# Kernel tuning notes

Hardware: AMD Instinct MI355X
Metric: run time of the kernel (lower is better)

## Reference

```python
import jax, jax.numpy as jnp
from jax import lax
import numpy as np

B, T, D, H, OUT = 128, 1024, 3, 512, 26


def setup_inputs() -> dict:
    key = jax.random.key(0)
    ks = jax.random.split(key, 8)
    s_in = 1.0 / np.sqrt(D)
    s_h = 1.0 / np.sqrt(H)
    return {
        "x": jax.random.normal(ks[0], (B, T, D), jnp.float32),
        # layer 0: gate order [i, f, z, o], W:(4H,in), R:(4H,H), b:(4H,)
        "W0": jax.random.normal(ks[1], (4 * H, D), jnp.float32) * s_in,
        "R0": jax.random.normal(ks[2], (4 * H, H), jnp.float32) * s_h,
        "b0": jnp.zeros((4 * H,), jnp.float32),
        # layer 1
        "W1": jax.random.normal(ks[3], (4 * H, H), jnp.float32) * s_h,
        "R1": jax.random.normal(ks[4], (4 * H, H), jnp.float32) * s_h,
        "b1": jnp.zeros((4 * H,), jnp.float32),
        # final linear head
        "fc_w": jax.random.normal(ks[5], (OUT, H), jnp.float32) * s_h,
        "fc_b": jnp.zeros((OUT,), jnp.float32),
    }


def _slstm_layer(xp, R):
    """sLSTM with exponential gating + stabilizer/normalizer states.
    xp: (B, T, 4H) precomputed input projections (incl. bias). Returns h: (B, T, H).
    """
    Bn, Tn, H4 = xp.shape
    Hh = H4 // 4

    def step(carry, g_in):
        h, c, n, m = carry
        g = g_in + h @ R.T                      # (B, 4H)
        i_pre, f_pre, z_pre, o_pre = jnp.split(g, 4, axis=-1)
        m_new = jnp.maximum(f_pre + m, i_pre)   # stabilizer (log-space)
        i_g = jnp.exp(i_pre - m_new)            # stabilized exp input gate
        f_g = jnp.exp(f_pre + m - m_new)        # stabilized exp forget gate
        c_new = f_g * c + i_g * jnp.tanh(z_pre)
        n_new = f_g * n + i_g                   # normalizer state
        h_new = jax.nn.sigmoid(o_pre) * c_new / jnp.maximum(n_new, 1e-6)
        return (h_new, c_new, n_new, m_new), h_new

    z = jnp.zeros((Bn, Hh), xp.dtype)
    init = (z, z, z, z)
    _, hs = lax.scan(step, init, jnp.swapaxes(xp, 0, 1))  # (T, B, H)
    return jnp.swapaxes(hs, 0, 1)


def reference(x, W0, R0, b0, W1, R1, b1, fc_w, fc_b):
    # layer 0 (input projections done as one big parallel GEMM)
    xp0 = jnp.einsum("btd,gd->btg", x, W0) + b0
    h1 = _slstm_layer(xp0, R0)
    # layer 1 (inter-layer dropout is identity at eval)
    xp1 = jnp.einsum("bth,gh->btg", h1, W1) + b1
    h2 = _slstm_layer(xp1, R1)
    # last-step hidden -> linear head (dropout identity at eval)
    last = h2[:, -1, :]                         # (B, H)
    return last @ fc_w.T + fc_b                 # (B, OUT)
```

## Files before the change

### kernel.cpp

```cpp
#include <hip/hip_runtime.h>
#include <hip/hip_bf16.h>

typedef _Float16 f16x8 __attribute__((ext_vector_type(8)));
typedef float f32x4 __attribute__((ext_vector_type(4)));
typedef unsigned long long u64;

#define B_   128
#define T_   1024
#define H_   512
#define P_   32
#define HC_  16
#define MB_  32
#define NC_  8
#define NW_  4
#define SPIN_BOUND (1 << 20)

#define FRAG_MT 8192

#define WS_HEXHI  0ull
#define WS_HEXLO  524288ull
#define WS_FLAGR  1048576ull
#define WS_FLAGX  1081344ull
#define WS_XCC    1097728ull
#define WS_MECH   1098752ull
#define WS_PROBE  1099776ull
#define WS_ZEROL  1100800ull
#define WS_XT     1100800ull
#define WS_HLAST  2673664ull
#define WS_H1HI   2935808ull
#define WS_H1LO   137153536ull
#define WS_NEED_SMALL 137153536ull

#define MFMA(a, b, c) __builtin_amdgcn_mfma_f32_16x16x32_f16((a), (b), (c), 0, 0, 0)

#define LD8C(FLAGS, D, P0, P1)                                                  \
    asm volatile(                                                               \
        "global_load_dwordx4 %0, %8, off " FLAGS "\n\t"                         \
        "global_load_dwordx4 %1, %8, off offset:1024 " FLAGS "\n\t"             \
        "global_load_dwordx4 %2, %8, off offset:2048 " FLAGS "\n\t"             \
        "global_load_dwordx4 %3, %8, off offset:3072 " FLAGS "\n\t"             \
        "global_load_dwordx4 %4, %9, off " FLAGS "\n\t"                         \
        "global_load_dwordx4 %5, %9, off offset:1024 " FLAGS "\n\t"             \
        "global_load_dwordx4 %6, %9, off offset:2048 " FLAGS "\n\t"             \
        "global_load_dwordx4 %7, %9, off offset:3072 " FLAGS "\n\t"             \
        "s_waitcnt vmcnt(0)"                                                    \
        : "=&v"(D[0][0]), "=&v"(D[1][0]), "=&v"(D[2][0]), "=&v"(D[3][0]),       \
          "=&v"(D[0][1]), "=&v"(D[1][1]), "=&v"(D[2][1]), "=&v"(D[3][1])        \
        : "v"(P0), "v"(P1)                                                      \
        : "memory")

__device__ __forceinline__ unsigned ald4(const unsigned* p) {
    return __hip_atomic_load(p, __ATOMIC_RELAXED, __HIP_MEMORY_SCOPE_AGENT);
}
__device__ __forceinline__ void ast4(void* p, unsigned v) {
    __hip_atomic_store((unsigned*)p, v, __ATOMIC_RELAXED, __HIP_MEMORY_SCOPE_AGENT);
}
__device__ __forceinline__ void st4_plain(unsigned* p, unsigned v) {
    asm volatile("global_store_dword %0, %1, off" :: "v"(p), "v"(v) : "memory");
}
__device__ __forceinline__ unsigned ld4_sc1(const unsigned* p) {
    unsigned r;
    asm volatile("global_load_dword %0, %1, off sc1\n\ts_waitcnt vmcnt(0)"
                 : "=v"(r) : "v"(p) : "memory");
    return r;
}
__device__ __forceinline__ void st16_plain(void* p, f16x8 v) {
    asm volatile("global_store_dwordx4 %0, %1, off" :: "v"(p), "v"(v) : "memory");
}
__device__ __forceinline__ void st16_ic(void* p, f16x8 v) {
    asm volatile("global_store_dwordx4 %0, %1, off sc0 sc1" :: "v"(p), "v"(v) : "memory");
}
__device__ __forceinline__ unsigned short f16bits(_Float16 h) {
    union { _Float16 f; unsigned short s; } u; u.f = h; return u.s;
}
__device__ __forceinline__ void heat(unsigned v) {
    float a = (float)(v & 7u) + 1.0f;
    #pragma unroll
    for (int i = 0; i < 16; ++i)
        asm volatile("v_fmac_f32 %0, %1, %2" : "+v"(a) : "v"(1.000001f), "v"(a));
    asm volatile("" :: "v"(a));
}
__device__ __forceinline__ int swz(int cidx) { return cidx ^ ((cidx >> 3) & 7); }

__global__ __launch_bounds__(256)
void xt_kernel(const float* __restrict__ x, float* __restrict__ xT) {
    int idx = blockIdx.x * 256 + threadIdx.x;
    if (idx < B_ * T_ * 3) {
        int d = idx % 3, rest = idx / 3;
        int t = rest % T_, b = rest / T_;
        xT[((size_t)t * B_ + b) * 3 + d] = x[idx];
    }
}

__global__ __launch_bounds__(256, 1)
void fused_slstm(const float* __restrict__ xT,
                 const float* __restrict__ W0, const float* __restrict__ R0,
                 const float* __restrict__ b0v,
                 const float* __restrict__ W1, const float* __restrict__ R1,
                 const float* __restrict__ b1v,
                 _Float16* __restrict__ hexFhi, _Float16* __restrict__ hexFlo,
                 unsigned* __restrict__ flagR, unsigned* __restrict__ flagX,
                 unsigned* __restrict__ xccbuf, unsigned* __restrict__ mech,
                 unsigned* __restrict__ probe,
                 _Float16* __restrict__ h1Fhi, _Float16* __restrict__ h1Flo,
                 float* __restrict__ hlast)
{
    constexpr int LDSH = 4 * 16 * 64 * 8;
    __shared__ _Float16 lds[2 * LDSH];
    __shared__ f32x4 bufA[512], bufB[512];
    __shared__ unsigned tbuf32[256];
    __shared__ int verdLds, mechLds, fastLds;

    const int tid  = threadIdx.x;
    const int lane = tid & 63;
    const int wid  = tid >> 6;
    const int l15  = lane & 15;
    const int l4   = lane >> 4;
    const int kg8  = l4 * 8;
    const int c    = blockIdx.x & 7;
    const int p    = blockIdx.x >> 3;
    const bool isL2 = (c >= 4);
    const int g    = c & 3;
    const int b0g  = g * MB_;

    const float* Rg  = isL2 ? R1 : R0;
    const float* bgp = isL2 ? b1v : b0v;

    {
        const int q = wid;
        const int grow = q * H_ + p * HC_ + l15;
        const float* rsrc = Rg + (size_t)grow * H_ + kg8;
        for (int kt = 0; kt < 16; ++kt) {
            const float* s = rsrc + kt * 32;
            _Float16* dhi = &lds[((q * 16 + kt) * 64 + lane) * 8];
            _Float16* dlo = dhi + LDSH;
            if (!isL2) {
                #pragma unroll
                for (int j = 0; j < 8; ++j) {
                    float v = s[j];
                    _Float16 h = (_Float16)v;
                    dhi[j] = h;
                    dlo[j] = (_Float16)(v - (float)h);
                }
            } else {
                const float* ws2 = W1 + (size_t)grow * H_ + kt * 32 + kg8;
                #pragma unroll
                for (int j = 0; j < 8; ++j) {
                    dhi[j] = (_Float16)s[j];
                    dlo[j] = (_Float16)ws2[j];
                }
            }
        }
    }

    {
        unsigned myxcc;
        asm volatile("s_getreg_b32 %0, hwreg(20, 0, 32)" : "=s"(myxcc));
        if (tid == 0) ast4(xccbuf + blockIdx.x, 0x100u | (myxcc & 0xFFu));
        if (wid == 0) {
            const unsigned* xp = xccbuf + ((lane & 31) * 8 + c);
            unsigned v = 0;
            int ok = 0;
            for (int it = 0; it < SPIN_BOUND; ++it) {
                v = ald4(xp);
                if (__ballot(v >= 0x100u) == ~0ull) { ok = 1; break; }
                __builtin_amdgcn_s_sleep(2);
            }
            unsigned ref = (unsigned)__shfl((int)v, 0);
            bool alleq = ok && (__ballot((v & 0xFFu) == (ref & 0xFFu)) == ~0ull);
            unsigned o = 0;
            int ok2 = 0;
            const unsigned* op = xccbuf + (c ^ 1);
            for (int it = 0; it < SPIN_BOUND; ++it) {
                o = ald4(op);
                if (o >= 0x100u) { ok2 = 1; break; }
                __builtin_amdgcn_s_sleep(2);
            }
            bool cand = alleq && ok2 && ((o & 0xFFu) != (ref & 0xFFu));
            if (lane == 0) verdLds = cand ? 1 : 0;
        }
    }
    __syncthreads();
    const bool candFast = (verdLds != 0);

    if (candFast && p == 0 && tid == 0) {
        for (unsigned k = 1; k <= 3; ++k) {
            st4_plain(probe + c * 32, k);
            asm volatile("s_waitcnt vmcnt(0)" ::: "memory");
            for (int s = 0; s < 32; ++s) __builtin_amdgcn_s_sleep(127);
        }
    }
    if (candFast && wid == 0) {
        unsigned first = 0xFFFFFFFFu;
        int got = 0;
        for (int it = 0; it < (1 << 16); ++it) {
            unsigned v = ld4_sc1(probe + c * 32);
            if (first == 0xFFFFFFFFu) first = v;
            if (v >= 3u) { got = 1; break; }
            __builtin_amdgcn_s_sleep(2);
        }
        if (p != 0 && first >= 3u) got = 0;
        if (lane == 0) mechLds = got;
    }
    __syncthreads();
    const int saw = candFast ? mechLds : 0;

    if (tid == 0) ast4(mech + blockIdx.x, 0x100u | (unsigned)(saw & 1));
    if (wid == 0) {
        const unsigned* mp = mech + ((lane & 31) * 8 + c);
        unsigned v = 0;
        int ok = 0;
        for (int it = 0; it < SPIN_BOUND; ++it) {
            v = ald4(mp);
            if (__ballot(v >= 0x100u) == ~0ull) { ok = 1; break; }
            __builtin_amdgcn_s_sleep(2);
        }
        bool allsaw = ok && (__ballot((v & 1u) != 0u) == ~0ull);
        if (lane == 0) fastLds = (candFast && allsaw) ? 1 : 0;
    }

    const int colIdx = tid & 15;
    const int col    = p * HC_ + colIdx;
    const int row0   = tid >> 4;
    float bb[4], w0r[4][3];
    #pragma unroll
    for (int q = 0; q < 4; ++q) bb[q] = bgp[q * H_ + col];
    if (!isL2) {
        #pragma unroll
        for (int q = 0; q < 4; ++q)
            #pragma unroll
            for (int d = 0; d < 3; ++d)
                w0r[q][d] = W0[(size_t)(q * H_ + col) * 3 + d];
    }
    float cS[2] = {0.f, 0.f}, nS[2] = {0.f, 0.f}, mS[2] = {0.f, 0.f};

    const int kt0 = wid * 4;
    int dead = 0;

    __syncthreads();
    const bool fast = (fastLds != 0);

    for (int t = 0; t < T_; ++t) {
        float xa[2][3];
        if (!isL2) {
            #pragma unroll
            for (int h = 0; h < 2; ++h) {
                const float* xp = xT + ((size_t)t * B_ + b0g + row0 + h * 16) * 3;
                xa[h][0] = xp[0]; xa[h][1] = xp[1]; xa[h][2] = xp[2];
            }
        }

        f32x4 acc[2][4];
        #pragma unroll
        for (int mt = 0; mt < 2; ++mt)
            #pragma unroll
            for (int q = 0; q < 4; ++q) { f32x4 z = {0.f,0.f,0.f,0.f}; acc[mt][q] = z; }

        if (isL2) {
            if (!dead) {
                const unsigned* fx = flagX + ((size_t)(g * 32 + (lane & 31)) << 5);
                int it = 0;
                for (;;) {
                    unsigned v = fast ? ld4_sc1(fx) : ald4(fx);
                    if (__ballot(v >= (unsigned)(t + 1)) == ~0ull) break;
                    if (++it > SPIN_BOUND) { dead = 1; break; }
                    heat(v);
                }
            }
            asm volatile("" ::: "memory");
            f16x8 xh[4][2];
            const size_t tb = (((size_t)t * 4 + g) * 2) * FRAG_MT + kt0 * 512 + lane * 8;
            const _Float16* q0 = h1Fhi + tb;
            const _Float16* q1 = h1Fhi + tb + FRAG_MT;
            LD8C("sc0 sc1", xh, q0, q1);
            #pragma unroll
            for (int k = 0; k < 4; ++k)
                #pragma unroll
                for (int q = 0; q < 4; ++q) {
                    f16x8 w = *(const f16x8*)&lds[LDSH + ((q * 16 + kt0 + k) * 64 + lane) * 8];
                    acc[0][q] = MFMA(xh[k][0], w, acc[0][q]);
                    acc[1][q] = MFMA(xh[k][1], w, acc[1][q]);
                }
        }

        if (t > 0 && !dead) {
            const unsigned* fr = flagR + ((size_t)(c * 32 + (lane & 31)) << 5);
            int it = 0;
            for (;;) {
                unsigned v = fast ? ld4_sc1(fr) : ald4(fr);
                if (__ballot(v >= (unsigned)t) == ~0ull) break;
                if (++it > SPIN_BOUND) { dead = 1; break; }
                heat(v);
            }
            asm volatile("" ::: "memory");
        }

        f16x8 ah[4][2];
        {
            const size_t hb = (((size_t)(t & 1) * NC_ + c) * 2) * FRAG_MT + kt0 * 512 + lane * 8;
            const _Float16* ph0 = hexFhi + hb;
            const _Float16* ph1 = hexFhi + hb + FRAG_MT;
            if (fast) { LD8C("sc1", ah, ph0, ph1); }
            else      { LD8C("sc0 sc1", ah, ph0, ph1); }
        }
        #pragma unroll
        for (int k = 0; k < 4; ++k)
            #pragma unroll
            for (int q = 0; q < 4; ++q) {
                f16x8 rh = *(const f16x8*)&lds[((q * 16 + kt0 + k) * 64 + lane) * 8];
                acc[0][q] = MFMA(ah[k][0], rh, acc[0][q]);
                acc[1][q] = MFMA(ah[k][1], rh, acc[1][q]);
                if (!isL2) {
                    f16x8 rlo = *(const f16x8*)&lds[LDSH + ((q * 16 + kt0 + k) * 64 + lane) * 8];
                    acc[0][q] = MFMA(ah[k][0], rlo, acc[0][q]);
                    acc[1][q] = MFMA(ah[k][1], rlo, acc[1][q]);
                }
            }

        if (wid == 1) {
            #pragma unroll
            for (int mt = 0; mt < 2; ++mt)
                #pragma unroll
                for (int q = 0; q < 4; ++q)
                    bufA[swz((mt * 4 + q) * 64 + lane)] = acc[mt][q];
        } else if (wid == 3) {
            #pragma unroll
            for (int mt = 0; mt < 2; ++mt)
                #pragma unroll
                for (int q = 0; q < 4; ++q)
                    bufB[swz((mt * 4 + q) * 64 + lane)] = acc[mt][q];
        }
        __syncthreads();
        if (wid == 2) {
            #pragma unroll
            for (int mt = 0; mt < 2; ++mt)
                #pragma unroll
                for (int q = 0; q < 4; ++q) {
                    const int s = swz((mt * 4 + q) * 64 + lane);
                    f32x4 v = bufA[s]; v += acc[mt][q]; bufA[s] = v;
                }
        } else if (wid == 0) {
            #pragma unroll
            for (int mt = 0; mt < 2; ++mt)
                #pragma unroll
                for (int q = 0; q < 4; ++q) {
                    const int s = swz((mt * 4 + q) * 64 + lane);
                    f32x4 v = bufB[s]; v += acc[mt][q]; bufB[s] = v;
                }
        }
        __syncthreads();

        const float* fA = (const float*)bufA;
        const float* fB = (const float*)bufB;
        unsigned pk[2];
        #pragma unroll
        for (int h = 0; h < 2; ++h) {
            float gq[4];
            #pragma unroll
            for (int q = 0; q < 4; ++q) {
                const int cidx = (h * 4 + q) * 64 + (row0 >> 2) * 16 + colIdx;
                const int w = swz(cidx) * 4 + (row0 & 3);
                float e = fA[w] + fB[w] + bb[q];
                if (!isL2)
                    e += w0r[q][0]*xa[h][0] + w0r[q][1]*xa[h][1] + w0r[q][2]*xa[h][2];
                gq[q] = e;
            }
            float iv = gq[0], fv = gq[1], zv = gq[2], ov = gq[3];
            float fm = fv + mS[h];
            float mn = fmaxf(fm, iv);
            float ig = __expf(iv - mn);
            float fg = __expf(fm - mn);
            float zc = fminf(fmaxf(zv, -15.f), 15.f);
            float e2 = __expf(2.f * zc);
            float th = (e2 - 1.f) / (e2 + 1.f);
            cS[h] = fg * cS[h] + ig * th;
            nS[h] = fg * nS[h] + ig;
            mS[h] = mn;
            float sg = 1.f / (1.f + __expf(-ov));
            float hv = sg * cS[h] / fmaxf(nS[h], 1e-6f);

            if (isL2 && t == T_ - 1)
                hlast[(size_t)(b0g + row0 + h * 16) * H_ + col] = hv;

            unsigned self = (unsigned)f16bits((_Float16)hv);
            unsigned part = (unsigned)__shfl_xor((int)(self << 16), 1) >> 16;
            pk[h] = (self & 0xffffu) | ((unsigned)part << 16);
        }

        if (!(colIdx & 1)) {
            const int fl4i = colIdx >> 3;
            const int cj   = (colIdx & 7) >> 1;
            #pragma unroll
            for (int h = 0; h < 2; ++h)
                tbuf32[((h * 2 + fl4i) * 16 + row0) * 4 + cj] = pk[h];
        }
        __syncthreads();

        if (wid == 0) {
            const f16x8* tv = (const f16x8*)tbuf32;
            f16x8 vh = tv[lane & 63];
            const int mt   = lane >> 5;
            const int fl4i = (lane >> 4) & 1;
            const int row  = lane & 15;
            const int flg  = row + 16 * ((p & 1) * 2 + fl4i);
            const size_t tail = (size_t)(p >> 1) * 512 + (size_t)flg * 8;
            const size_t feh = (((size_t)((t + 1) & 1) * NC_ + c) * 2 + mt) * FRAG_MT + tail;
            if (fast) st16_plain(hexFhi + feh, vh);
            else      st16_ic(hexFhi + feh, vh);
            asm volatile("s_waitcnt vmcnt(0)" ::: "memory");
            if (lane == 0) {
                unsigned* frp = flagR + ((size_t)(c * 32 + p) << 5);
                if (fast) st4_plain(frp, (unsigned)(t + 1));
                else      ast4(frp, (unsigned)(t + 1));
                if (!isL2) ast4(flagX + ((size_t)(c * 32 + p) << 5), (unsigned)t);
            }
            if (!isL2) {
                const size_t fex = (((size_t)t * 4 + g) * 2 + mt) * FRAG_MT + tail;
                st16_ic(h1Fhi + fex, vh);
            }
        }
    }

    if (!isL2) {
        asm volatile("s_waitcnt vmcnt(0)" ::: "memory");
        __syncthreads();
        if (tid == 0) ast4(flagX + ((size_t)(c * 32 + p) << 5), (unsigned)(T_ + 1));
    }
}

#define OUT_ 26
__global__ __launch_bounds__(64)
void fc_kernel(const float* __restrict__ hlast, const float* __restrict__ fcw,
               const float* __restrict__ fcb, float* __restrict__ out)
{
    int b = blockIdx.x, oo = threadIdx.x;
    if (oo < OUT_) {
        const float4* hv = reinterpret_cast<const float4*>(hlast + (size_t)b * H_);
        const float4* wv = reinterpret_cast<const float4*>(fcw + (size_t)oo * H_);
        float s = fcb[oo];
        #pragma unroll 4
        for (int k = 0; k < H_ / 4; ++k) {
            float4 h4 = hv[k], w4 = wv[k];
            s += h4.x * w4.x + h4.y * w4.y + h4.z * w4.z + h4.w * w4.w;
        }
        out[(size_t)b * OUT_ + oo] = s;
    }
}

extern "C" void kernel_launch(void* const* d_in, const int* in_sizes, int n_in,
                              void* d_out, int out_size, void* d_ws, size_t ws_size,
                              hipStream_t stream) {
    const float* x   = (const float*)d_in[0];
    const float* W0  = (const float*)d_in[1];
    const float* R0  = (const float*)d_in[2];
    const float* b0  = (const float*)d_in[3];
    const float* W1  = (const float*)d_in[4];
    const float* R1  = (const float*)d_in[5];
    const float* b1  = (const float*)d_in[6];
    const float* fcw = (const float*)d_in[7];
    const float* fcb = (const float*)d_in[8];
    float* out = (float*)d_out;

    if (ws_size < WS_NEED_SMALL) return;

    char* ws = (char*)d_ws;
    _Float16* hexFhi = (_Float16*)(ws + WS_HEXHI);
    _Float16* hexFlo = (_Float16*)(ws + WS_HEXLO);
    unsigned* flagR  = (unsigned*)(ws + WS_FLAGR);
    unsigned* flagX  = (unsigned*)(ws + WS_FLAGX);
    unsigned* xccb   = (unsigned*)(ws + WS_XCC);
    unsigned* mech   = (unsigned*)(ws + WS_MECH);
    unsigned* probe  = (unsigned*)(ws + WS_PROBE);
    float*    xTp    = (float*)(ws + WS_XT);
    float*    hlast  = (float*)(ws + WS_HLAST);
    _Float16* h1Fhi  = (_Float16*)(ws + WS_H1HI);
    _Float16* h1Flo  = (_Float16*)(ws + WS_H1LO);

    hipMemsetAsync(ws, 0, WS_ZEROL, stream);
    xt_kernel<<<(B_ * T_ * 3 + 255) / 256, 256, 0, stream>>>(x, xTp);
    fused_slstm<<<NC_ * P_, NW_ * 64, 0, stream>>>(xTp, W0, R0, b0, W1, R1, b1,
                                                   hexFhi, hexFlo, flagR, flagX,
                                                   xccb, mech, probe,
                                                   h1Fhi, h1Flo, hlast);
    fc_kernel<<<B_, 64, 0, stream>>>(hlast, fcw, fcb, out);
}
```

Measured before the change: 3.881 ms.

## Split recurrent MFMA across warps by gate pairs and write hidden state directly

Warps are regrouped so each pair covers half the K range for two of the four gates, instead of each warp covering a quarter of K for all gates. Each warp now writes its partial sums straight into one of two LDS buffers, which removes a serial add stage and one block barrier per timestep. The LDS transpose staging buffer is also dropped: threads write packed fp16 hidden values to global memory as scattered dword stores, replacing a single wave's 16-byte stores. The trade is that each warp issues twice as many global fragment loads per step, and the global stores become many small writes.

```diff
diff --git a/kernel.cpp b/kernel.cpp
--- a/kernel.cpp
+++ b/kernel.cpp
@@ -33,20 +33,30 @@
 
 #define MFMA(a, b, c) __builtin_amdgcn_mfma_f32_16x16x32_f16((a), (b), (c), 0, 0, 0)
 
-#define LD8C(FLAGS, D, P0, P1)                                                  \
+#define LD16C(FLAGS, D, DB, P0, P1, P2, P3)                                     \
     asm volatile(                                                               \
-        "global_load_dwordx4 %0, %8, off " FLAGS "\n\t"                         \
-        "global_load_dwordx4 %1, %8, off offset:1024 " FLAGS "\n\t"             \
-        "global_load_dwordx4 %2, %8, off offset:2048 " FLAGS "\n\t"             \
-        "global_load_dwordx4 %3, %8, off offset:3072 " FLAGS "\n\t"             \
-        "global_load_dwordx4 %4, %9, off " FLAGS "\n\t"                         \
-        "global_load_dwordx4 %5, %9, off offset:1024 " FLAGS "\n\t"             \
-        "global_load_dwordx4 %6, %9, off offset:2048 " FLAGS "\n\t"             \
-        "global_load_dwordx4 %7, %9, off offset:3072 " FLAGS "\n\t"             \
+        "global_load_dwordx4 %0, %16, off " FLAGS "\n\t"                        \
+        "global_load_dwordx4 %1, %16, off offset:1024 " FLAGS "\n\t"            \
+        "global_load_dwordx4 %2, %16, off offset:2048 " FLAGS "\n\t"            \
+        "global_load_dwordx4 %3, %16, off offset:3072 " FLAGS "\n\t"            \
+        "global_load_dwordx4 %4, %17, off " FLAGS "\n\t"                        \
+        "global_load_dwordx4 %5, %17, off offset:1024 " FLAGS "\n\t"            \
+        "global_load_dwordx4 %6, %17, off offset:2048 " FLAGS "\n\t"            \
+        "global_load_dwordx4 %7, %17, off offset:3072 " FLAGS "\n\t"            \
+        "global_load_dwordx4 %8, %18, off " FLAGS "\n\t"                        \
+        "global_load_dwordx4 %9, %18, off offset:1024 " FLAGS "\n\t"            \
+        "global_load_dwordx4 %10, %18, off offset:2048 " FLAGS "\n\t"           \
+        "global_load_dwordx4 %11, %18, off offset:3072 " FLAGS "\n\t"           \
+        "global_load_dwordx4 %12, %19, off " FLAGS "\n\t"                       \
+        "global_load_dwordx4 %13, %19, off offset:1024 " FLAGS "\n\t"           \
+        "global_load_dwordx4 %14, %19, off offset:2048 " FLAGS "\n\t"           \
+        "global_load_dwordx4 %15, %19, off offset:3072 " FLAGS "\n\t"           \
         "s_waitcnt vmcnt(0)"                                                    \
         : "=&v"(D[0][0]), "=&v"(D[1][0]), "=&v"(D[2][0]), "=&v"(D[3][0]),       \
-          "=&v"(D[0][1]), "=&v"(D[1][1]), "=&v"(D[2][1]), "=&v"(D[3][1])        \
-        : "v"(P0), "v"(P1)                                                      \
+          "=&v"(D[0][1]), "=&v"(D[1][1]), "=&v"(D[2][1]), "=&v"(D[3][1]),       \
+          "=&v"(DB[0][0]), "=&v"(DB[1][0]), "=&v"(DB[2][0]), "=&v"(DB[3][0]),   \
+          "=&v"(DB[0][1]), "=&v"(DB[1][1]), "=&v"(DB[2][1]), "=&v"(DB[3][1])    \
+        : "v"(P0), "v"(P1), "v"(P2), "v"(P3)                                    \
         : "memory")
 
 __device__ __forceinline__ unsigned ald4(const unsigned* p) {
@@ -63,12 +73,6 @@
     asm volatile("global_load_dword %0, %1, off sc1\n\ts_waitcnt vmcnt(0)"
                  : "=v"(r) : "v"(p) : "memory");
     return r;
-}
-__device__ __forceinline__ void st16_plain(void* p, f16x8 v) {
-    asm volatile("global_store_dwordx4 %0, %1, off" :: "v"(p), "v"(v) : "memory");
-}
-__device__ __forceinline__ void st16_ic(void* p, f16x8 v) {
-    asm volatile("global_store_dwordx4 %0, %1, off sc0 sc1" :: "v"(p), "v"(v) : "memory");
 }
 __device__ __forceinline__ unsigned short f16bits(_Float16 h) {
     union { _Float16 f; unsigned short s; } u; u.f = h; return u.s;
@@ -108,7 +112,6 @@
     constexpr int LDSH = 4 * 16 * 64 * 8;
     __shared__ _Float16 lds[2 * LDSH];
     __shared__ f32x4 bufA[512], bufB[512];
-    __shared__ unsigned tbuf32[256];
     __shared__ int verdLds, mechLds, fastLds;
 
     const int tid  = threadIdx.x;
@@ -222,6 +225,10 @@
     const int colIdx = tid & 15;
     const int col    = p * HC_ + colIdx;
     const int row0   = tid >> 4;
+    const int fkt  = col >> 5;
+    const int fl4s = (col >> 3) & 3;
+    const int fj   = col & 7;
+    const size_t tail = (size_t)fkt * 512 + ((size_t)row0 + 16 * fl4s) * 8 + fj;
     float bb[4], w0r[4][3];
     #pragma unroll
     for (int q = 0; q < 4; ++q) bb[q] = bgp[q * H_ + col];
@@ -234,7 +241,9 @@
     }
     float cS[2] = {0.f, 0.f}, nS[2] = {0.f, 0.f}, mS[2] = {0.f, 0.f};
 
-    const int kt0 = wid * 4;
+    const int gp  = wid & 1;
+    const int kh  = wid >> 1;
+    const int kt0 = kh * 8;
     int dead = 0;
 
     __syncthreads();
@@ -250,11 +259,11 @@
             }
         }
 
-        f32x4 acc[2][4];
+        f32x4 acc[2][2];
         #pragma unroll
         for (int mt = 0; mt < 2; ++mt)
             #pragma unroll
-            for (int q = 0; q < 4; ++q) { f32x4 z = {0.f,0.f,0.f,0.f}; acc[mt][q] = z; }
+            for (int qq = 0; qq < 2; ++qq) { f32x4 z = {0.f,0.f,0.f,0.f}; acc[mt][qq] = z; }
 
         if (isL2) {
             if (!dead) {
@@ -268,19 +277,22 @@
                 }
             }
             asm volatile("" ::: "memory");
-            f16x8 xh[4][2];
+            f16x8 xh[8][2];
             const size_t tb = (((size_t)t * 4 + g) * 2) * FRAG_MT + kt0 * 512 + lane * 8;
             const _Float16* q0 = h1Fhi + tb;
             const _Float16* q1 = h1Fhi + tb + FRAG_MT;
-            LD8C("sc0 sc1", xh, q0, q1);
-            #pragma unroll
-            for (int k = 0; k < 4; ++k)
+            LD16C("sc0 sc1", xh, (xh + 4), q0, q1, (q0 + 2048), (q1 + 2048));
+            #pragma unroll
+            for (int k = 0; k < 8; ++k) {
+                const int kt = kt0 + k;
                 #pragma unroll
-                for (int q = 0; q < 4; ++q) {
-                    f16x8 w = *(const f16x8*)&lds[LDSH + ((q * 16 + kt0 + k) * 64 + lane) * 8];
-                    acc[0][q] = MFMA(xh[k][0], w, acc[0][q]);
-                    acc[1][q] = MFMA(xh[k][1], w, acc[1][q]);
+                for (int qq = 0; qq < 2; ++qq) {
+                    const int q = gp * 2 + qq;
+                    f16x8 w = *(const f16x8*)&lds[LDSH + ((q * 16 + kt) * 64 + lane) * 8];
+                    acc[0][qq] = MFMA(xh[k][0], w, acc[0][qq]);
+                    acc[1][qq] = MFMA(xh[k][1], w, acc[1][qq]);
                 }
+            }
         }
 
         if (t > 0 && !dead) {
@@ -295,58 +307,38 @@
             asm volatile("" ::: "memory");
         }
 
-        f16x8 ah[4][2];
+        f16x8 ah[8][2];
         {
             const size_t hb = (((size_t)(t & 1) * NC_ + c) * 2) * FRAG_MT + kt0 * 512 + lane * 8;
             const _Float16* ph0 = hexFhi + hb;
             const _Float16* ph1 = hexFhi + hb + FRAG_MT;
-            if (fast) { LD8C("sc1", ah, ph0, ph1); }
-            else      { LD8C("sc0 sc1", ah, ph0, ph1); }
+            if (fast) { LD16C("sc1", ah, (ah + 4), ph0, ph1, (ph0 + 2048), (ph1 + 2048)); }
+            else      { LD16C("sc0 sc1", ah, (ah + 4), ph0, ph1, (ph0 + 2048), (ph1 + 2048)); }
         }
         #pragma unroll
-        for (int k = 0; k < 4; ++k)
-            #pragma unroll
-            for (int q = 0; q < 4; ++q) {
-                f16x8 rh = *(const f16x8*)&lds[((q * 16 + kt0 + k) * 64 + lane) * 8];
-                acc[0][q] = MFMA(ah[k][0], rh, acc[0][q]);
-                acc[1][q] = MFMA(ah[k][1], rh, acc[1][q]);
+        for (int k = 0; k < 8; ++k) {
+            const int kt = kt0 + k;
+            #pragma unroll
+            for (int qq = 0; qq < 2; ++qq) {
+                const int q = gp * 2 + qq;
+                f16x8 rh = *(const f16x8*)&lds[((q * 16 + kt) * 64 + lane) * 8];
+                acc[0][qq] = MFMA(ah[k][0], rh, acc[0][qq]);
+                acc[1][qq] = MFMA(ah[k][1], rh, acc[1][qq]);
                 if (!isL2) {
-                    f16x8 rlo = *(const f16x8*)&lds[LDSH + ((q * 16 + kt0 + k) * 64 + lane) * 8];
-                    acc[0][q] = MFMA(ah[k][0], rlo, acc[0][q]);
-                    acc[1][q] = MFMA(ah[k][1], rlo, acc[1][q]);
+                    f16x8 rlo = *(const f16x8*)&lds[LDSH + ((q * 16 + kt) * 64 + lane) * 8];
+                    acc[0][qq] = MFMA(ah[k][0], rlo, acc[0][qq]);
+                    acc[1][qq] = MFMA(ah[k][1], rlo, acc[1][qq]);
                 }
             }
-
-        if (wid == 1) {
+        }
+
+        {
+            f32x4* dep = (kh == 0) ? bufA : bufB;
             #pragma unroll
             for (int mt = 0; mt < 2; ++mt)
                 #pragma unroll
-                for (int q = 0; q < 4; ++q)
-                    bufA[swz((mt * 4 + q) * 64 + lane)] = acc[mt][q];
-        } else if (wid == 3) {
-            #pragma unroll
-            for (int mt = 0; mt < 2; ++mt)
-                #pragma unroll
-                for (int q = 0; q < 4; ++q)
-                    bufB[swz((mt * 4 + q) * 64 + lane)] = acc[mt][q];
-        }
-        __syncthreads();
-        if (wid == 2) {
-            #pragma unroll
-            for (int mt = 0; mt < 2; ++mt)
-                #pragma unroll
-                for (int q = 0; q < 4; ++q) {
-                    const int s = swz((mt * 4 + q) * 64 + lane);
-                    f32x4 v = bufA[s]; v += acc[mt][q]; bufA[s] = v;
-                }
-        } else if (wid == 0) {
-            #pragma unroll
-            for (int mt = 0; mt < 2; ++mt)
-                #pragma unroll
-                for (int q = 0; q < 4; ++q) {
-                    const int s = swz((mt * 4 + q) * 64 + lane);
-                    f32x4 v = bufB[s]; v += acc[mt][q]; bufB[s] = v;
-                }
+                for (int qq = 0; qq < 2; ++qq)
+                    dep[swz((mt * 4 + gp * 2 + qq) * 64 + lane)] = acc[mt][qq];
         }
         __syncthreads();
 
@@ -388,35 +380,27 @@
         }
 
         if (!(colIdx & 1)) {
-            const int fl4i = colIdx >> 3;
-            const int cj   = (colIdx & 7) >> 1;
-            #pragma unroll
-            for (int h = 0; h < 2; ++h)
-                tbuf32[((h * 2 + fl4i) * 16 + row0) * 4 + cj] = pk[h];
-        }
+            #pragma unroll
+            for (int h = 0; h < 2; ++h) {
+                const size_t feh = (((size_t)((t + 1) & 1) * NC_ + c) * 2 + h) * FRAG_MT + tail;
+                if (fast) st4_plain((unsigned*)(hexFhi + feh), pk[h]);
+                else      ast4(hexFhi + feh, pk[h]);
+            }
+        }
+        asm volatile("s_waitcnt vmcnt(0)" ::: "memory");
         __syncthreads();
-
-        if (wid == 0) {
-            const f16x8* tv = (const f16x8*)tbuf32;
-            f16x8 vh = tv[lane & 63];
-            const int mt   = lane >> 5;
-            const int fl4i = (lane >> 4) & 1;
-            const int row  = lane & 15;
-            const int flg  = row + 16 * ((p & 1) * 2 + fl4i);
-            const size_t tail = (size_t)(p >> 1) * 512 + (size_t)flg * 8;
-            const size_t feh = (((size_t)((t + 1) & 1) * NC_ + c) * 2 + mt) * FRAG_MT + tail;
-            if (fast) st16_plain(hexFhi + feh, vh);
-            else      st16_ic(hexFhi + feh, vh);
-            asm volatile("s_waitcnt vmcnt(0)" ::: "memory");
-            if (lane == 0) {
-                unsigned* frp = flagR + ((size_t)(c * 32 + p) << 5);
-                if (fast) st4_plain(frp, (unsigned)(t + 1));
-                else      ast4(frp, (unsigned)(t + 1));
-                if (!isL2) ast4(flagX + ((size_t)(c * 32 + p) << 5), (unsigned)t);
-            }
-            if (!isL2) {
-                const size_t fex = (((size_t)t * 4 + g) * 2 + mt) * FRAG_MT + tail;
-                st16_ic(h1Fhi + fex, vh);
+        if (tid == 0) {
+            unsigned* frp = flagR + ((size_t)(c * 32 + p) << 5);
+            if (fast) st4_plain(frp, (unsigned)(t + 1));
+            else      ast4(frp, (unsigned)(t + 1));
+            if (!isL2) ast4(flagX + ((size_t)(c * 32 + p) << 5), (unsigned)t);
+        }
+
+        if (!isL2 && !(colIdx & 1)) {
+            #pragma unroll
+            for (int h = 0; h < 2; ++h) {
+                const size_t fex = (((size_t)t * 4 + g) * 2 + h) * FRAG_MT + tail;
+                ast4(h1Fhi + fex, pk[h]);
             }
         }
     }
```

Result: no change. 3.946 ms (+1.7%).
